# Optimization experiments

Hardware: AMD Instinct MI355X
Metric: run time of the kernel (lower is better)

Reference implementation:

```python
import jax, jax.numpy as jnp
import numpy as np

THRESH = 0.2  # contact probability threshold from _make_graph default


def setup_inputs() -> dict:
    key = jax.random.key(0)
    ks = jax.random.split(key, 10)
    L, D, K, M = 1024, 640, 32, 64
    S = jax.random.normal(ks[0], (L, D), jnp.float32)
    P = jax.random.uniform(ks[1], (L, L), jnp.float32)
    P = 0.5 * (P + P.T)  # symmetric base-pair probability matrix
    xyz = jax.random.normal(ks[2], (L, 3), jnp.float32) * 10.0  # Angstrom-scale C1' coords
    rbf_mu = jnp.linspace(0.0, 30.0, K).astype(jnp.float32)     # RBF centers over 0-30 A
    rbf_sigma = jax.random.uniform(ks[3], (K,), jnp.float32, 0.5, 2.0)
    W_edge = jax.random.normal(ks[4], (K + 2, M), jnp.float32) * 0.05
    b_edge = jnp.zeros((M,), jnp.float32)
    W_node = jax.random.normal(ks[5], (D, M), jnp.float32) * 0.05
    w_out = jax.random.normal(ks[6], (M,), jnp.float32) * 0.1
    return {"S": S, "P": P, "xyz": xyz, "rbf_mu": rbf_mu, "rbf_sigma": rbf_sigma,
            "W_edge": W_edge, "b_edge": b_edge, "W_node": W_node, "w_out": w_out}


def reference(S, P, xyz, rbf_mu, rbf_sigma, W_edge, b_edge, W_node, w_out):
    """Graph construction (_make_graph) + one SE3-style gated coordinate update.

    Edges: backbone (j == i+1, etype=0, pij=1) and high-prob contacts
    (P[i,j] > THRESH, j > i+2, etype=1, pij=P[i,j]). Edge scalars are
    [etype, pij, rbf(d)] exactly as in _make_graph; edge vectors are
    xyz[j]-xyz[i]. Computed in dense masked form for jit-compatibility.
    """
    L = xyz.shape[0]
    rel = xyz[None, :, :] - xyz[:, None, :]                      # (L,L,3) xyz[j]-xyz[i]
    # safe norm: eps avoids nan grad on zero diagonal (diagonal is masked out anyway)
    d = jnp.sqrt(jnp.sum(rel * rel, axis=-1, keepdims=True) + 1e-12)  # (L,L,1)
    rbf_feat = jnp.exp(-(d - rbf_mu) ** 2 / (2.0 * rbf_sigma ** 2))   # (L,L,K)

    idx = jnp.arange(L)
    backbone = idx[None, :] == idx[:, None] + 1                  # j == i+1
    contact = (P > THRESH) & (idx[None, :] > idx[:, None] + 2)   # skip j <= i+2
    mask = backbone | contact                                    # (L,L)

    etype = contact.astype(S.dtype)                              # 0 backbone, 1 contact
    pij = jnp.where(backbone, jnp.asarray(1.0, S.dtype), P)
    e_scalar = jnp.concatenate([etype[..., None], pij[..., None], rbf_feat], axis=-1)  # (L,L,K+2)

    # gather-compute: message from edge scalars + destination-node scalars
    node_proj = S @ W_node                                       # (L,M)
    msg = jax.nn.relu(jnp.einsum('ijk,km->ijm', e_scalar, W_edge) + b_edge
                      + node_proj[None, :, :])                   # (L,L,M)
    gate = jax.nn.sigmoid(msg @ w_out) * mask.astype(S.dtype)    # (L,L)

    # scatter: equivariant coordinate update, sum of gated edge vectors per node
    xyz_out = xyz + jnp.einsum('ij,ijc->ic', gate, rel)          # (L,3)
    return xyz_out
```

## Files before the change

kernel.cpp:

```cpp
#include <hip/hip_runtime.h>
#include <math.h>

#define LL 1024
#define DD 640
#define KK 32
#define MM 64
#define THRESH 0.2f
#define LOG2E 1.4426950408889634f

#define NPROJ_OFF  0
#define NPROJC_OFF (NPROJ_OFF + LL * MM)
#define WRT_OFF    (NPROJC_OFF + LL * MM)
#define W1_OFF     (WRT_OFF + 1024)
#define EA_OFF     (W1_OFF + MM)
#define EB_OFF     (EA_OFF + KK)
#define EC_OFF     (EB_OFF + KK)
#define XYZ4_OFF   (EC_OFF + KK)

typedef float f32x4_t __attribute__((ext_vector_type(4)));
typedef short bf16x8_t __attribute__((ext_vector_type(8)));

union FragU { unsigned int u[4]; bf16x8_t v; };

#if __has_builtin(__builtin_amdgcn_sqrtf)
#define FSQRT __builtin_amdgcn_sqrtf
#else
#define FSQRT sqrtf
#endif

#if __has_builtin(__builtin_amdgcn_exp2f)
#define EXP2F __builtin_amdgcn_exp2f
#else
#define EXP2F(x) __expf((x) * 0.6931471805599453f)
#endif

__device__ __forceinline__ unsigned int pack_bf(float hi, float lo) {
    return __builtin_amdgcn_perm(__float_as_uint(hi), __float_as_uint(lo), 0x07060302u);
}

__global__ __launch_bounds__(256) void prep_gemm(
    const float* __restrict__ S, const float* __restrict__ xyz,
    const float* __restrict__ rbf_mu, const float* __restrict__ rbf_sigma,
    const float* __restrict__ W_edge, const float* __restrict__ b_edge,
    const float* __restrict__ W_node, float* __restrict__ ws,
    float* __restrict__ out)
{
    const int b = blockIdx.x;
    const int t = threadIdx.x;
    if (b < 64) {
        const int lane = t & 63;
        const int wave = t >> 6;
        const int id   = b * 4 + wave;
        const int r0   = (id >> 2) * 16;
        const int n0   = (id & 3) * 16;
        const int col  = lane & 15;
        const int quad = lane >> 4;

        f32x4_t acc = {0.f, 0.f, 0.f, 0.f};
        const float* arow = S + (size_t)(r0 + col) * DD + quad * 8;
        const float* bcol = W_node + (size_t)(quad * 8) * MM + n0 + col;

        #pragma unroll 2
        for (int ks = 0; ks < 20; ++ks) {
            const float4 a0 = *(const float4*)(arow + ks * 32);
            const float4 a1 = *(const float4*)(arow + ks * 32 + 4);
            FragU A;
            A.u[0] = pack_bf(a0.y, a0.x); A.u[1] = pack_bf(a0.w, a0.z);
            A.u[2] = pack_bf(a1.y, a1.x); A.u[3] = pack_bf(a1.w, a1.z);
            const float* bk = bcol + (size_t)ks * 32 * MM;
            const float b0 = bk[0 * MM], b1 = bk[1 * MM], b2 = bk[2 * MM], b3 = bk[3 * MM];
            const float b4 = bk[4 * MM], b5 = bk[5 * MM], b6 = bk[6 * MM], b7 = bk[7 * MM];
            FragU B;
            B.u[0] = pack_bf(b1, b0); B.u[1] = pack_bf(b3, b2);
            B.u[2] = pack_bf(b5, b4); B.u[3] = pack_bf(b7, b6);
            acc = __builtin_amdgcn_mfma_f32_16x16x32_bf16(A.v, B.v, acc, 0, 0, 0);
        }
        const float bias = b_edge[n0 + col];
        const float w0   = W_edge[n0 + col];
        #pragma unroll
        for (int r = 0; r < 4; ++r) {
            const int row = r0 + quad * 4 + r;
            const float v = acc[r] + bias;
            ws[NPROJ_OFF  + (size_t)row * MM + n0 + col] = v;
            ws[NPROJC_OFF + (size_t)row * MM + n0 + col] = v + w0;
        }
    } else {
        unsigned short* wrt = (unsigned short*)(ws + WRT_OFF);
        if (t < MM) ws[W1_OFF + t] = W_edge[MM + t];
        if (t < KK) {
            const float s  = rbf_sigma[t];
            const float m_ = rbf_mu[t];
            const float inv = 1.0f / (2.0f * s * s);
            ws[EA_OFF + t] = -LOG2E * inv;
            ws[EB_OFF + t] =  2.0f * LOG2E * inv * m_;
            ws[EC_OFF + t] = -LOG2E * inv * m_ * m_;
        }
        for (int idx = t; idx < KK * MM; idx += 256) {
            const int m = idx >> 5, k = idx & 31;
            unsigned int u = __float_as_uint(W_edge[(2 + k) * MM + m]);
            u = (u + 0x7fffu + ((u >> 16) & 1u)) >> 16;
            wrt[idx] = (unsigned short)u;
        }
        for (int n = t; n < LL; n += 256) {
            float4 v;
            v.x = xyz[3 * n + 0]; v.y = xyz[3 * n + 1];
            v.z = xyz[3 * n + 2]; v.w = 0.0f;
            *(float4*)(ws + XYZ4_OFF + 4 * n) = v;
        }
        for (int idx = t; idx < 3 * LL; idx += 256) out[idx] = xyz[idx];
    }
}

__global__ __launch_bounds__(256, 4) void edge_kernel2(
    const float* __restrict__ P, const float* __restrict__ w_out,
    const float* __restrict__ ws, float* __restrict__ out)
{
    const int tid  = threadIdx.x;
    const int lane = tid & 63;
    const int wave = tid >> 6;
    const int quad = lane >> 4;
    const int col  = lane & 15;
    __shared__ float sred[4][3];

    const float* __restrict__ nproj  = ws + NPROJ_OFF;
    const float* __restrict__ nprojc = ws + NPROJC_OFF;
    const float4* __restrict__ xyz4  = (const float4*)(ws + XYZ4_OFF);
    const unsigned short* __restrict__ wrt = (const unsigned short*)(ws + WRT_OFF);

    FragU ar[4];
    float w1r[16], wvr[16];
    float aj[8], bj[8], cj[8];
    #pragma unroll
    for (int mt = 0; mt < 4; ++mt) {
        const uint4 w = *(const uint4*)(wrt + (mt * 16 + col) * KK + quad * 8);
        ar[mt].u[0] = w.x; ar[mt].u[1] = w.y; ar[mt].u[2] = w.z; ar[mt].u[3] = w.w;
        const f32x4_t w1 = *(const f32x4_t*)(ws + W1_OFF + mt * 16 + quad * 4);
        const f32x4_t wo = *(const f32x4_t*)(w_out + mt * 16 + quad * 4);
        #pragma unroll
        for (int r = 0; r < 4; ++r) { w1r[mt * 4 + r] = w1[r]; wvr[mt * 4 + r] = wo[r]; }
    }
    #pragma unroll
    for (int j = 0; j < 8; ++j) {
        aj[j] = ws[EA_OFF + quad * 8 + j];
        bj[j] = ws[EB_OFF + quad * 8 + j];
        cj[j] = ws[EC_OFF + quad * 8 + j];
    }
    #pragma unroll
    for (int mt = 0; mt < 4; ++mt) {
        asm volatile("" : "+v"(ar[mt].u[0]), "+v"(ar[mt].u[1]),
                          "+v"(ar[mt].u[2]), "+v"(ar[mt].u[3]));
        asm volatile("" : "+v"(w1r[mt*4+0]), "+v"(w1r[mt*4+1]),
                          "+v"(w1r[mt*4+2]), "+v"(w1r[mt*4+3]));
        asm volatile("" : "+v"(wvr[mt*4+0]), "+v"(wvr[mt*4+1]),
                          "+v"(wvr[mt*4+2]), "+v"(wvr[mt*4+3]));
    }
    #pragma unroll
    for (int j = 0; j < 8; j += 4) {
        asm volatile("" : "+v"(aj[j]), "+v"(aj[j+1]), "+v"(aj[j+2]), "+v"(aj[j+3]));
        asm volatile("" : "+v"(bj[j]), "+v"(bj[j+1]), "+v"(bj[j+2]), "+v"(bj[j+3]));
        asm volatile("" : "+v"(cj[j]), "+v"(cj[j+1]), "+v"(cj[j+2]), "+v"(cj[j+3]));
    }

    const int g = (int)blockIdx.x;
    const int i = g >> 1;
    const int h = g & 1;
    const float4 xo = xyz4[i];
    const float xi0 = xo.x, xi1 = xo.y, xi2 = xo.z;
    const int len = (LL - 1) - i;
    float ax = 0.f, ay = 0.f, az = 0.f;
    const float* __restrict__ prow = P + (size_t)i * LL;

    const int b0 = (h * 4 + wave) * 64;

    float pp[4];
    #pragma unroll
    for (int ct = 0; ct < 4; ++ct) {
        int jc = i + 1 + b0 + ct * 16 + col;
        jc = (jc < LL) ? jc : (LL - 1);
        pp[ct] = prow[jc];
    }

    for (int base = b0; base < len; base += 512) {
        float pc[4];
        #pragma unroll
        for (int ct = 0; ct < 4; ++ct) pc[ct] = pp[ct];
        #pragma unroll
        for (int ct = 0; ct < 4; ++ct) {
            int jc = i + 1 + base + 512 + ct * 16 + col;
            jc = (jc < LL) ? jc : (LL - 1);
            pp[ct] = prow[jc];
        }

        const int jo = base + lane;
        const bool valid = jo < len;
        const int jc_o = valid ? (i + 1 + jo) : (LL - 1);
        const float4 xj = xyz4[jc_o];
        const float rx = xj.x - xi0, ry = xj.y - xi1, rz = xj.z - xi2;
        float p_own = pc[0];
        p_own = (quad == 1) ? pc[1] : p_own;
        p_own = (quad == 2) ? pc[2] : p_own;
        p_own = (quad == 3) ? pc[3] : p_own;
        const bool msk = valid && ((jo == 0) || ((jo >= 2) && (p_own > THRESH)));

        float res[4];
        #pragma unroll
        for (int ct = 0; ct < 4; ++ct) {
            const int jo_n = base + ct * 16 + col;
            int jc_n = i + 1 + jo_n;
            jc_n = (jc_n < LL) ? jc_n : (LL - 1);
            const float4 xn = xyz4[jc_n];
            const float dx = xn.x - xi0, dy = xn.y - xi1, dz = xn.z - xi2;
            const float d_n = FSQRT(fmaf(dx, dx, fmaf(dy, dy, fmaf(dz, dz, 1e-12f))));
            const float d2 = d_n * d_n;
            const bool bb = (jo_n == 0);
            const float peff = bb ? 1.0f : pc[ct];
            const float* npr = (bb ? nproj : nprojc) + (size_t)jc_n * MM;

            float e[8];
            #pragma unroll
            for (int j = 0; j < 8; ++j)
                e[j] = EXP2F(fmaf(aj[j], d2, fmaf(bj[j], d_n, cj[j])));
            FragU bf;
            bf.u[0] = pack_bf(e[1], e[0]); bf.u[1] = pack_bf(e[3], e[2]);
            bf.u[2] = pack_bf(e[5], e[4]); bf.u[3] = pack_bf(e[7], e[6]);

            float gg = 0.0f;
            #pragma unroll
            for (int mt = 0; mt < 4; ++mt) {
                f32x4_t c0 = *(const f32x4_t*)(npr + mt * 16 + quad * 4);
                c0[0] = fmaf(peff, w1r[mt*4+0], c0[0]);
                c0[1] = fmaf(peff, w1r[mt*4+1], c0[1]);
                c0[2] = fmaf(peff, w1r[mt*4+2], c0[2]);
                c0[3] = fmaf(peff, w1r[mt*4+3], c0[3]);
                c0 = __builtin_amdgcn_mfma_f32_16x16x32_bf16(ar[mt].v, bf.v, c0, 0, 0, 0);
                gg = fmaf(fmaxf(c0[0], 0.f), wvr[mt*4+0], gg);
                gg = fmaf(fmaxf(c0[1], 0.f), wvr[mt*4+1], gg);
                gg = fmaf(fmaxf(c0[2], 0.f), wvr[mt*4+2], gg);
                gg = fmaf(fmaxf(c0[3], 0.f), wvr[mt*4+3], gg);
            }
            gg += __shfl_xor(gg, 16, 64);
            gg += __shfl_xor(gg, 32, 64);
            res[ct] = gg;
        }
        float gd = res[0];
        gd = (quad == 1) ? res[1] : gd;
        gd = (quad == 2) ? res[2] : gd;
        gd = (quad == 3) ? res[3] : gd;
        const float gate = msk ? (1.0f / (1.0f + __expf(-gd))) : 0.0f;
        ax = fmaf(gate, rx, ax);
        ay = fmaf(gate, ry, ay);
        az = fmaf(gate, rz, az);
    }

    #pragma unroll
    for (int off = 32; off > 0; off >>= 1) {
        ax += __shfl_down(ax, off, 64);
        ay += __shfl_down(ay, off, 64);
        az += __shfl_down(az, off, 64);
    }
    if (lane == 0) { sred[wave][0] = ax; sred[wave][1] = ay; sred[wave][2] = az; }
    __syncthreads();
    if (tid == 0) {
        const float tx = (sred[0][0] + sred[1][0]) + (sred[2][0] + sred[3][0]);
        const float ty = (sred[0][1] + sred[1][1]) + (sred[2][1] + sred[3][1]);
        const float tz = (sred[0][2] + sred[1][2]) + (sred[2][2] + sred[3][2]);
        atomicAdd(out + i * 3 + 0, tx);
        atomicAdd(out + i * 3 + 1, ty);
        atomicAdd(out + i * 3 + 2, tz);
    }
}

extern "C" void kernel_launch(void* const* d_in, const int* in_sizes, int n_in,
                              void* d_out, int out_size, void* d_ws, size_t ws_size,
                              hipStream_t stream) {
    const float* S         = (const float*)d_in[0];
    const float* P         = (const float*)d_in[1];
    const float* xyz       = (const float*)d_in[2];
    const float* rbf_mu    = (const float*)d_in[3];
    const float* rbf_sigma = (const float*)d_in[4];
    const float* W_edge    = (const float*)d_in[5];
    const float* b_edge    = (const float*)d_in[6];
    const float* W_node    = (const float*)d_in[7];
    const float* w_out     = (const float*)d_in[8];
    float* out = (float*)d_out;
    float* ws  = (float*)d_ws;

    prep_gemm<<<65, 256, 0, stream>>>(S, xyz, rbf_mu, rbf_sigma,
                                      W_edge, b_edge, W_node, ws, out);
    edge_kernel2<<<2 * LL, 256, 0, stream>>>(P, w_out, ws, out);
}
```

Before: 105.6 us.

## Use one block per row with batched MFMA tiles and direct output writes

Each row is now handled by one block instead of two half-rows, so the final sum is written directly as xyz plus the delta rather than with atomics, and the output initialisation copy is dropped from the prep kernel. The inner loop now computes all four column tiles' RBF features first, then issues four independent MFMAs per weight tile, to raise instruction-level parallelism. This also removes the register-pinning asm barriers, the P prefetch and the 4-waves occupancy bound. The cost is higher register pressure and half as many blocks, which may hurt load balance on the triangular workload.

```diff
diff --git a/kernel.cpp b/kernel.cpp
--- a/kernel.cpp
+++ b/kernel.cpp
@@ -42,8 +42,7 @@
     const float* __restrict__ S, const float* __restrict__ xyz,
     const float* __restrict__ rbf_mu, const float* __restrict__ rbf_sigma,
     const float* __restrict__ W_edge, const float* __restrict__ b_edge,
-    const float* __restrict__ W_node, float* __restrict__ ws,
-    float* __restrict__ out)
+    const float* __restrict__ W_node, float* __restrict__ ws)
 {
     const int b = blockIdx.x;
     const int t = threadIdx.x;
@@ -107,11 +106,10 @@
             v.z = xyz[3 * n + 2]; v.w = 0.0f;
             *(float4*)(ws + XYZ4_OFF + 4 * n) = v;
         }
-        for (int idx = t; idx < 3 * LL; idx += 256) out[idx] = xyz[idx];
-    }
-}
-
-__global__ __launch_bounds__(256, 4) void edge_kernel2(
+    }
+}
+
+__global__ __launch_bounds__(256) void edge_kernel3(
     const float* __restrict__ P, const float* __restrict__ w_out,
     const float* __restrict__ ws, float* __restrict__ out)
 {
@@ -145,107 +143,97 @@
         bj[j] = ws[EB_OFF + quad * 8 + j];
         cj[j] = ws[EC_OFF + quad * 8 + j];
     }
-    #pragma unroll
-    for (int mt = 0; mt < 4; ++mt) {
-        asm volatile("" : "+v"(ar[mt].u[0]), "+v"(ar[mt].u[1]),
-                          "+v"(ar[mt].u[2]), "+v"(ar[mt].u[3]));
-        asm volatile("" : "+v"(w1r[mt*4+0]), "+v"(w1r[mt*4+1]),
-                          "+v"(w1r[mt*4+2]), "+v"(w1r[mt*4+3]));
-        asm volatile("" : "+v"(wvr[mt*4+0]), "+v"(wvr[mt*4+1]),
-                          "+v"(wvr[mt*4+2]), "+v"(wvr[mt*4+3]));
-    }
-    #pragma unroll
-    for (int j = 0; j < 8; j += 4) {
-        asm volatile("" : "+v"(aj[j]), "+v"(aj[j+1]), "+v"(aj[j+2]), "+v"(aj[j+3]));
-        asm volatile("" : "+v"(bj[j]), "+v"(bj[j+1]), "+v"(bj[j+2]), "+v"(bj[j+3]));
-        asm volatile("" : "+v"(cj[j]), "+v"(cj[j+1]), "+v"(cj[j+2]), "+v"(cj[j+3]));
-    }
-
-    const int g = (int)blockIdx.x;
-    const int i = g >> 1;
-    const int h = g & 1;
+
+    const int i = (int)blockIdx.x;
     const float4 xo = xyz4[i];
     const float xi0 = xo.x, xi1 = xo.y, xi2 = xo.z;
     const int len = (LL - 1) - i;
     float ax = 0.f, ay = 0.f, az = 0.f;
     const float* __restrict__ prow = P + (size_t)i * LL;
 
-    const int b0 = (h * 4 + wave) * 64;
-
-    float pp[4];
-    #pragma unroll
-    for (int ct = 0; ct < 4; ++ct) {
-        int jc = i + 1 + b0 + ct * 16 + col;
-        jc = (jc < LL) ? jc : (LL - 1);
-        pp[ct] = prow[jc];
-    }
-
-    for (int base = b0; base < len; base += 512) {
-        float pc[4];
-        #pragma unroll
-        for (int ct = 0; ct < 4; ++ct) pc[ct] = pp[ct];
+    for (int base = wave * 64; base < len; base += 256) {
+        float pcv[4], dnv[4], q2v[4], dxv[4], dyv[4], dzv[4];
+        const float* npr[4];
+        float peff[4];
         #pragma unroll
         for (int ct = 0; ct < 4; ++ct) {
-            int jc = i + 1 + base + 512 + ct * 16 + col;
+            const int jo_n = base + ct * 16 + col;
+            int jc = i + 1 + jo_n;
             jc = (jc < LL) ? jc : (LL - 1);
-            pp[ct] = prow[jc];
+            pcv[ct] = prow[jc];
+            const float4 xn = xyz4[jc];
+            dxv[ct] = xn.x - xi0; dyv[ct] = xn.y - xi1; dzv[ct] = xn.z - xi2;
+            q2v[ct] = fmaf(dxv[ct], dxv[ct],
+                      fmaf(dyv[ct], dyv[ct],
+                      fmaf(dzv[ct], dzv[ct], 1e-12f)));
+            dnv[ct] = FSQRT(q2v[ct]);
+            const bool bb = (jo_n == 0);
+            peff[ct] = bb ? 1.0f : pcv[ct];
+            npr[ct] = (bb ? nproj : nprojc) + (size_t)jc * MM;
         }
 
         const int jo = base + lane;
         const bool valid = jo < len;
-        const int jc_o = valid ? (i + 1 + jo) : (LL - 1);
-        const float4 xj = xyz4[jc_o];
-        const float rx = xj.x - xi0, ry = xj.y - xi1, rz = xj.z - xi2;
-        float p_own = pc[0];
-        p_own = (quad == 1) ? pc[1] : p_own;
-        p_own = (quad == 2) ? pc[2] : p_own;
-        p_own = (quad == 3) ? pc[3] : p_own;
+        float rx = dxv[0], ry = dyv[0], rz = dzv[0], p_own = pcv[0];
+        rx = (quad == 1) ? dxv[1] : rx; rx = (quad == 2) ? dxv[2] : rx; rx = (quad == 3) ? dxv[3] : rx;
+        ry = (quad == 1) ? dyv[1] : ry; ry = (quad == 2) ? dyv[2] : ry; ry = (quad == 3) ? dyv[3] : ry;
+        rz = (quad == 1) ? dzv[1] : rz; rz = (quad == 2) ? dzv[2] : rz; rz = (quad == 3) ? dzv[3] : rz;
+        p_own = (quad == 1) ? pcv[1] : p_own;
+        p_own = (quad == 2) ? pcv[2] : p_own;
+        p_own = (quad == 3) ? pcv[3] : p_own;
         const bool msk = valid && ((jo == 0) || ((jo >= 2) && (p_own > THRESH)));
 
-        float res[4];
+        float e[4][8];
+        #pragma unroll
+        for (int ct = 0; ct < 4; ++ct)
+            #pragma unroll
+            for (int j = 0; j < 8; ++j)
+                e[ct][j] = EXP2F(fmaf(aj[j], q2v[ct], fmaf(bj[j], dnv[ct], cj[j])));
+
+        FragU bf[4];
         #pragma unroll
         for (int ct = 0; ct < 4; ++ct) {
-            const int jo_n = base + ct * 16 + col;
-            int jc_n = i + 1 + jo_n;
-            jc_n = (jc_n < LL) ? jc_n : (LL - 1);
-            const float4 xn = xyz4[jc_n];
-            const float dx = xn.x - xi0, dy = xn.y - xi1, dz = xn.z - xi2;
-            const float d_n = FSQRT(fmaf(dx, dx, fmaf(dy, dy, fmaf(dz, dz, 1e-12f))));
-            const float d2 = d_n * d_n;
-            const bool bb = (jo_n == 0);
-            const float peff = bb ? 1.0f : pc[ct];
-            const float* npr = (bb ? nproj : nprojc) + (size_t)jc_n * MM;
-
-            float e[8];
-            #pragma unroll
-            for (int j = 0; j < 8; ++j)
-                e[j] = EXP2F(fmaf(aj[j], d2, fmaf(bj[j], d_n, cj[j])));
-            FragU bf;
-            bf.u[0] = pack_bf(e[1], e[0]); bf.u[1] = pack_bf(e[3], e[2]);
-            bf.u[2] = pack_bf(e[5], e[4]); bf.u[3] = pack_bf(e[7], e[6]);
-
-            float gg = 0.0f;
-            #pragma unroll
-            for (int mt = 0; mt < 4; ++mt) {
-                f32x4_t c0 = *(const f32x4_t*)(npr + mt * 16 + quad * 4);
-                c0[0] = fmaf(peff, w1r[mt*4+0], c0[0]);
-                c0[1] = fmaf(peff, w1r[mt*4+1], c0[1]);
-                c0[2] = fmaf(peff, w1r[mt*4+2], c0[2]);
-                c0[3] = fmaf(peff, w1r[mt*4+3], c0[3]);
-                c0 = __builtin_amdgcn_mfma_f32_16x16x32_bf16(ar[mt].v, bf.v, c0, 0, 0, 0);
-                gg = fmaf(fmaxf(c0[0], 0.f), wvr[mt*4+0], gg);
-                gg = fmaf(fmaxf(c0[1], 0.f), wvr[mt*4+1], gg);
-                gg = fmaf(fmaxf(c0[2], 0.f), wvr[mt*4+2], gg);
-                gg = fmaf(fmaxf(c0[3], 0.f), wvr[mt*4+3], gg);
+            bf[ct].u[0] = pack_bf(e[ct][1], e[ct][0]);
+            bf[ct].u[1] = pack_bf(e[ct][3], e[ct][2]);
+            bf[ct].u[2] = pack_bf(e[ct][5], e[ct][4]);
+            bf[ct].u[3] = pack_bf(e[ct][7], e[ct][6]);
+        }
+
+        float g[4] = {0.f, 0.f, 0.f, 0.f};
+        #pragma unroll
+        for (int mt = 0; mt < 4; ++mt) {
+            f32x4_t c[4];
+            #pragma unroll
+            for (int ct = 0; ct < 4; ++ct)
+                c[ct] = *(const f32x4_t*)(npr[ct] + mt * 16 + quad * 4);
+            #pragma unroll
+            for (int ct = 0; ct < 4; ++ct) {
+                c[ct][0] = fmaf(peff[ct], w1r[mt*4+0], c[ct][0]);
+                c[ct][1] = fmaf(peff[ct], w1r[mt*4+1], c[ct][1]);
+                c[ct][2] = fmaf(peff[ct], w1r[mt*4+2], c[ct][2]);
+                c[ct][3] = fmaf(peff[ct], w1r[mt*4+3], c[ct][3]);
             }
-            gg += __shfl_xor(gg, 16, 64);
-            gg += __shfl_xor(gg, 32, 64);
-            res[ct] = gg;
-        }
-        float gd = res[0];
-        gd = (quad == 1) ? res[1] : gd;
-        gd = (quad == 2) ? res[2] : gd;
-        gd = (quad == 3) ? res[3] : gd;
+            #pragma unroll
+            for (int ct = 0; ct < 4; ++ct)
+                c[ct] = __builtin_amdgcn_mfma_f32_16x16x32_bf16(ar[mt].v, bf[ct].v, c[ct], 0, 0, 0);
+            #pragma unroll
+            for (int ct = 0; ct < 4; ++ct) {
+                g[ct] = fmaf(fmaxf(c[ct][0], 0.f), wvr[mt*4+0], g[ct]);
+                g[ct] = fmaf(fmaxf(c[ct][1], 0.f), wvr[mt*4+1], g[ct]);
+                g[ct] = fmaf(fmaxf(c[ct][2], 0.f), wvr[mt*4+2], g[ct]);
+                g[ct] = fmaf(fmaxf(c[ct][3], 0.f), wvr[mt*4+3], g[ct]);
+            }
+        }
+
+        #pragma unroll
+        for (int ct = 0; ct < 4; ++ct) g[ct] += __shfl_xor(g[ct], 16, 64);
+        #pragma unroll
+        for (int ct = 0; ct < 4; ++ct) g[ct] += __shfl_xor(g[ct], 32, 64);
+
+        float gd = g[0];
+        gd = (quad == 1) ? g[1] : gd;
+        gd = (quad == 2) ? g[2] : gd;
+        gd = (quad == 3) ? g[3] : gd;
         const float gate = msk ? (1.0f / (1.0f + __expf(-gd))) : 0.0f;
         ax = fmaf(gate, rx, ax);
         ay = fmaf(gate, ry, ay);
@@ -264,9 +252,9 @@
         const float tx = (sred[0][0] + sred[1][0]) + (sred[2][0] + sred[3][0]);
         const float ty = (sred[0][1] + sred[1][1]) + (sred[2][1] + sred[3][1]);
         const float tz = (sred[0][2] + sred[1][2]) + (sred[2][2] + sred[3][2]);
-        atomicAdd(out + i * 3 + 0, tx);
-        atomicAdd(out + i * 3 + 1, ty);
-        atomicAdd(out + i * 3 + 2, tz);
+        out[i * 3 + 0] = xi0 + tx;
+        out[i * 3 + 1] = xi1 + ty;
+        out[i * 3 + 2] = xi2 + tz;
     }
 }
 
@@ -286,6 +274,6 @@
     float* ws  = (float*)d_ws;
 
     prep_gemm<<<65, 256, 0, stream>>>(S, xyz, rbf_mu, rbf_sigma,
-                                      W_edge, b_edge, W_node, ws, out);
-    edge_kernel2<<<2 * LL, 256, 0, stream>>>(P, w_out, ws, out);
-}
+                                      W_edge, b_edge, W_node, ws);
+    edge_kernel3<<<LL, 256, 0, stream>>>(P, w_out, ws, out);
+}
```

Measured after the change: 99.44 us. 1.06x faster.
